# Performance work log

Hardware: AMD Instinct MI355X
Metric: run time of the kernel (lower is better)

The kernel has to match this reference:

```python
import jax, jax.numpy as jnp
import numpy as np

NUM_WIRES = 4
NUM_LAYERS = 2
BATCH = 1_048_576


def _rz(theta):
    # diag(e^{-i t/2}, e^{+i t/2})
    e = jnp.exp(-0.5j * theta.astype(jnp.complex64))
    z = jnp.zeros((), jnp.complex64)
    return jnp.stack([jnp.stack([e, z]), jnp.stack([z, jnp.conj(e)])])


def _rx(theta):
    c = jnp.cos(0.5 * theta).astype(jnp.complex64)
    s = (-1j * jnp.sin(0.5 * theta)).astype(jnp.complex64)
    return jnp.stack([jnp.stack([c, s]), jnp.stack([s, c])])


def _apply_1q(state, U, w):
    # state: (B,2,2,2,2); apply 2x2 unitary U on wire w (axis w+1)
    s = jnp.moveaxis(state, w + 1, -1)
    s = jnp.einsum('...i,ji->...j', s, U)
    return jnp.moveaxis(s, -1, w + 1)


def _cnot(state, c, t):
    # flip target axis where control bit == 1
    s = jnp.moveaxis(state, (c + 1, t + 1), (-2, -1))
    s = jnp.stack([s[..., 0, :], s[..., 1, ::-1]], axis=-2)
    return jnp.moveaxis(s, (-2, -1), (c + 1, t + 1))


def _circuit(x, params):
    # RY(x_i)|0> per wire gives product state [cos(x_i/2), sin(x_i/2)]
    h = 0.5 * x
    a = jnp.stack([jnp.cos(h), jnp.sin(h)], axis=-1).astype(jnp.complex64)  # (B,4,2)
    state = jnp.einsum('bi,bj,bk,bl->bijkl', a[:, 0], a[:, 1], a[:, 2], a[:, 3])
    for layer in range(NUM_LAYERS):
        for w in range(NUM_WIRES):
            # RZ then RX on wire w, fused into one 2x2 unitary
            U = _rx(params[layer, w, 1]) @ _rz(params[layer, w, 0])
            state = _apply_1q(state, U, w)
        for w in range(NUM_WIRES - 1):
            state = _cnot(state, w, w + 1)
        state = _cnot(state, NUM_WIRES - 1, 0)
    probs = state.real ** 2 + state.imag ** 2  # (B,2,2,2,2)
    evs = []
    for w in range(NUM_WIRES):
        axes = tuple(ax for ax in range(1, NUM_WIRES + 1) if ax != w + 1)
        p = jnp.sum(probs, axis=axes)  # (B,2) marginal of wire w
        evs.append(p[:, 0] - p[:, 1])  # <Z_w>
    return jnp.stack(evs, axis=-1)  # (B,4)


def setup_inputs() -> dict:
    key = jax.random.key(0)
    k1, k2 = jax.random.split(key)
    x = jax.random.normal(k1, (BATCH, NUM_WIRES), dtype=jnp.float32)
    params = jax.random.normal(k2, (NUM_LAYERS, NUM_WIRES, 2), dtype=jnp.float32)
    return {"x": x, "params": params}


def reference(x, params):
    return _circuit(x, params)
```

## Files before the change

kernel.cpp:

```cpp
#include <hip/hip_runtime.h>
#include <math.h>

#define PI_F 3.14159265358979323846f


typedef __attribute__((address_space(4))) const float cfloat;

__global__ void gate_prep(const float* __restrict__ params, float* __restrict__ g) {
    __shared__ float L[324];
    const int tid = threadIdx.x;

    if (tid < 81) {
        const int t3 = tid % 3, t2 = (tid / 3) % 3, t1 = (tid / 9) % 3, t0 = tid / 27;
        const float xg[3] = {0.f, PI_F, 0.5f * PI_F};
        const float xs[4] = {xg[t0], xg[t1], xg[t2], xg[t3]};

        float zr[16], zi[16];
        {
            float c[4], s[4];
            for (int k = 0; k < 4; ++k) { c[k] = cosf(0.5f * xs[k]); s[k] = sinf(0.5f * xs[k]); }
            for (int i = 0; i < 16; ++i) {
                zr[i] = ((i & 8) ? s[0] : c[0]) * ((i & 4) ? s[1] : c[1]) *
                        ((i & 2) ? s[2] : c[2]) * ((i & 1) ? s[3] : c[3]);
                zi[i] = 0.f;
            }
        }
        for (int layer = 0; layer < 2; ++layer) {
            for (int w = 0; w < 4; ++w) {
                const float p0 = params[(layer * 4 + w) * 2 + 0];
                const float p1 = params[(layer * 4 + w) * 2 + 1];
                const float cz = cosf(0.5f * p0), sz = sinf(0.5f * p0);
                const float cx = cosf(0.5f * p1), sx = sinf(0.5f * p1);
                const float u00r = cx * cz,  u00i = -cx * sz;
                const float u01r = sx * sz,  u01i = -sx * cz;
                const float u10r = -sx * sz, u10i = -sx * cz;
                const float u11r = cx * cz,  u11i = cx * sz;
                const int M = 8 >> w;
                for (int i = 0; i < 16; ++i) {
                    if (!(i & M)) {
                        const int j = i | M;
                        const float ar = zr[i], ai = zi[i], br = zr[j], bi = zi[j];
                        zr[i] = u00r * ar - u00i * ai + u01r * br - u01i * bi;
                        zi[i] = u00r * ai + u00i * ar + u01r * bi + u01i * br;
                        zr[j] = u10r * ar - u10i * ai + u11r * br - u11i * bi;
                        zi[j] = u10r * ai + u10i * ar + u11r * bi + u11i * br;
                    }
                }
            }
            const int cm[4] = {8, 4, 2, 1}, tmm[4] = {4, 2, 1, 8};
            for (int kk = 0; kk < 4; ++kk)
                for (int i = 0; i < 16; ++i)
                    if ((i & cm[kk]) && !(i & tmm[kk])) {
                        const int j = i | tmm[kk];
                        float t;
                        t = zr[i]; zr[i] = zr[j]; zr[j] = t;
                        t = zi[i]; zi[i] = zi[j]; zi[j] = t;
                    }
        }
        float p[16];
        for (int i = 0; i < 16; ++i) p[i] = zr[i] * zr[i] + zi[i] * zi[i];
        const int wm[4] = {8, 4, 2, 1};
        for (int w = 0; w < 4; ++w) {
            float e = 0.f;
            for (int i = 0; i < 16; ++i) e += (i & wm[w]) ? -p[i] : p[i];
            L[w * 81 + tid] = e;
        }
    }
    __syncthreads();

    const int strides[4] = {27, 9, 3, 1};
    for (int d = 0; d < 4; ++d) {
        const int S = strides[d];
        if (tid < 108) {
            const int w = tid & 3, grp = tid >> 2;
            const int base = w * 81 + (grp / S) * (3 * S) + (grp % S);
            const float v0 = L[base], v1 = L[base + S], v2 = L[base + 2 * S];
            const float a0 = 0.5f * (v0 + v1);
            const float a1 = 0.5f * (v0 - v1);
            L[base] = a0;
            L[base + S] = a1;
            L[base + 2 * S] = v2 - a0;
        }
        __syncthreads();
    }

    for (int k = tid; k < 324; k += blockDim.x) {
        g[k] = L[(k & 3) * 81 + (k >> 2)];
    }
}

__global__ __launch_bounds__(256) void qsim_kernel(const float* __restrict__ x,
                                                   const float* __restrict__ gf,
                                                   float* __restrict__ out, int batch) {
    const int b = blockIdx.x * 256 + threadIdx.x;
    if (b >= batch) return;

    cfloat* T = (cfloat*)gf;

    const float4 xv = reinterpret_cast<const float4*>(x)[b];
    float c[4], s[4];
    __sincosf(xv.x, &s[0], &c[0]);
    __sincosf(xv.y, &s[1], &c[1]);
    __sincosf(xv.z, &s[2], &c[2]);
    __sincosf(xv.w, &s[3], &c[3]);

    float u[9];
    u[1] = c[3];        u[2] = s[3];
    u[3] = c[2];        u[6] = s[2];
    u[4] = c[2] * c[3]; u[5] = c[2] * s[3];
    u[7] = s[2] * c[3]; u[8] = s[2] * s[3];

    float ev[4];
#pragma unroll
    for (int t0 = 0; t0 < 3; ++t0) {
        float o1[4];
#pragma unroll
        for (int t1 = 0; t1 < 3; ++t1) {
            cfloat* Tp = T + (t0 * 3 + t1) * 36;
            float inner[4];
#pragma unroll
            for (int w = 0; w < 4; ++w) inner[w] = Tp[w];
#pragma unroll
            for (int p = 1; p < 9; ++p)
#pragma unroll
                for (int w = 0; w < 4; ++w)
                    inner[w] = fmaf(u[p], Tp[p * 4 + w], inner[w]);

            if (t1 == 0) {
#pragma unroll
                for (int w = 0; w < 4; ++w) o1[w] = inner[w];
            } else if (t1 == 1) {
#pragma unroll
                for (int w = 0; w < 4; ++w) o1[w] = fmaf(c[1], inner[w], o1[w]);
            } else {
#pragma unroll
                for (int w = 0; w < 4; ++w) o1[w] = fmaf(s[1], inner[w], o1[w]);
            }
        }
        if (t0 == 0) {
#pragma unroll
            for (int w = 0; w < 4; ++w) ev[w] = o1[w];
        } else if (t0 == 1) {
#pragma unroll
            for (int w = 0; w < 4; ++w) ev[w] = fmaf(c[0], o1[w], ev[w]);
        } else {
#pragma unroll
            for (int w = 0; w < 4; ++w) ev[w] = fmaf(s[0], o1[w], ev[w]);
        }
    }

    reinterpret_cast<float4*>(out)[b] = make_float4(ev[0], ev[1], ev[2], ev[3]);
}

extern "C" void kernel_launch(void* const* d_in, const int* in_sizes, int n_in,
                              void* d_out, int out_size, void* d_ws, size_t ws_size,
                              hipStream_t stream) {
    const float* x = (const float*)d_in[0];
    const float* params = (const float*)d_in[1];
    float* out = (float*)d_out;
    float* g = (float*)d_ws;
    const int batch = in_sizes[0] / 4;

    gate_prep<<<1, 128, 0, stream>>>(params, g);
    const int blocks = (batch + 255) / 256;
    qsim_kernel<<<blocks, 256, 0, stream>>>(x, g, out, batch);
}
```

Measured before the change: 89.65 us.

## Process two batch elements per thread and loop over tensor blocks with vector loads

Each thread now evaluates two samples, so every coefficient of the precomputed 324-float tensor it reads is used for two FMAs instead of one. The fully unrolled 9-block contraction becomes a non-unrolled loop that loads each 36-float block as float4 vectors through ordinary global pointers instead of constant-address-space scalar loads. This is meant to cut coefficient load traffic and instruction count per sample. In exchange it launches half as many blocks, adds loop overhead and per-iteration weight selects, and raises register use.

Result: no change. 90.41 us (+0.9%).

```diff
diff --git a/kernel.cpp b/kernel.cpp
--- a/kernel.cpp
+++ b/kernel.cpp
@@ -3,8 +3,6 @@
 
 #define PI_F 3.14159265358979323846f
 
-
-typedef __attribute__((address_space(4))) const float cfloat;
 
 __global__ void gate_prep(const float* __restrict__ params, float* __restrict__ g) {
     __shared__ float L[324];
@@ -90,66 +88,86 @@
 }
 
 __global__ __launch_bounds__(256) void qsim_kernel(const float* __restrict__ x,
-                                                   const float* __restrict__ gf,
+                                                   const float* __restrict__ T,
                                                    float* __restrict__ out, int batch) {
-    const int b = blockIdx.x * 256 + threadIdx.x;
-    if (b >= batch) return;
+    const int tid = threadIdx.x;
+    const int i0 = blockIdx.x * 512 + tid;
+    const int i1 = i0 + 256;
 
-    cfloat* T = (cfloat*)gf;
+    const float4 xa = (i0 < batch) ? reinterpret_cast<const float4*>(x)[i0]
+                                   : make_float4(0.f, 0.f, 0.f, 0.f);
+    const float4 xb = (i1 < batch) ? reinterpret_cast<const float4*>(x)[i1]
+                                   : make_float4(0.f, 0.f, 0.f, 0.f);
 
-    const float4 xv = reinterpret_cast<const float4*>(x)[b];
-    float c[4], s[4];
-    __sincosf(xv.x, &s[0], &c[0]);
-    __sincosf(xv.y, &s[1], &c[1]);
-    __sincosf(xv.z, &s[2], &c[2]);
-    __sincosf(xv.w, &s[3], &c[3]);
+    float cA[4], sA[4], cB[4], sB[4];
+    __sincosf(xa.x, &sA[0], &cA[0]);
+    __sincosf(xa.y, &sA[1], &cA[1]);
+    __sincosf(xa.z, &sA[2], &cA[2]);
+    __sincosf(xa.w, &sA[3], &cA[3]);
+    __sincosf(xb.x, &sB[0], &cB[0]);
+    __sincosf(xb.y, &sB[1], &cB[1]);
+    __sincosf(xb.z, &sB[2], &cB[2]);
+    __sincosf(xb.w, &sB[3], &cB[3]);
 
-    float u[9];
-    u[1] = c[3];        u[2] = s[3];
-    u[3] = c[2];        u[6] = s[2];
-    u[4] = c[2] * c[3]; u[5] = c[2] * s[3];
-    u[7] = s[2] * c[3]; u[8] = s[2] * s[3];
+    float uA[9], uB[9];
+    uA[1] = cA[3];          uA[2] = sA[3];
+    uA[3] = cA[2];          uA[6] = sA[2];
+    uA[4] = cA[2] * cA[3];  uA[5] = cA[2] * sA[3];
+    uA[7] = sA[2] * cA[3];  uA[8] = sA[2] * sA[3];
+    uB[1] = cB[3];          uB[2] = sB[3];
+    uB[3] = cB[2];          uB[6] = sB[2];
+    uB[4] = cB[2] * cB[3];  uB[5] = cB[2] * sB[3];
+    uB[7] = sB[2] * cB[3];  uB[8] = sB[2] * sB[3];
 
-    float ev[4];
+    float evA[4] = {0.f, 0.f, 0.f, 0.f};
+    float evB[4] = {0.f, 0.f, 0.f, 0.f};
+
+    const float* Tp = T;
+    int t0 = 0, t1 = 0;
+#pragma clang loop unroll(disable)
+    for (int q = 0; q < 9; ++q) {
+        float Tc[36];
 #pragma unroll
-    for (int t0 = 0; t0 < 3; ++t0) {
-        float o1[4];
+        for (int k = 0; k < 9; ++k) {
+            const float4 v = reinterpret_cast<const float4*>(Tp)[k];
+            Tc[4 * k + 0] = v.x;
+            Tc[4 * k + 1] = v.y;
+            Tc[4 * k + 2] = v.z;
+            Tc[4 * k + 3] = v.w;
+        }
+
+        float inA[4], inB[4];
 #pragma unroll
-        for (int t1 = 0; t1 < 3; ++t1) {
-            cfloat* Tp = T + (t0 * 3 + t1) * 36;
-            float inner[4];
+        for (int w = 0; w < 4; ++w) { inA[w] = Tc[w]; inB[w] = Tc[w]; }
 #pragma unroll
-            for (int w = 0; w < 4; ++w) inner[w] = Tp[w];
+        for (int p = 1; p < 9; ++p)
 #pragma unroll
-            for (int p = 1; p < 9; ++p)
+            for (int w = 0; w < 4; ++w) {
+                inA[w] = fmaf(uA[p], Tc[p * 4 + w], inA[w]);
+                inB[w] = fmaf(uB[p], Tc[p * 4 + w], inB[w]);
+            }
+
+        const float w0A = (t0 == 0) ? 1.0f : ((t0 == 1) ? cA[0] : sA[0]);
+        const float w1A = (t1 == 0) ? 1.0f : ((t1 == 1) ? cA[1] : sA[1]);
+        const float w0B = (t0 == 0) ? 1.0f : ((t0 == 1) ? cB[0] : sB[0]);
+        const float w1B = (t1 == 0) ? 1.0f : ((t1 == 1) ? cB[1] : sB[1]);
+        const float wA = w0A * w1A;
+        const float wB = w0B * w1B;
+
 #pragma unroll
-                for (int w = 0; w < 4; ++w)
-                    inner[w] = fmaf(u[p], Tp[p * 4 + w], inner[w]);
+        for (int w = 0; w < 4; ++w) {
+            evA[w] = fmaf(wA, inA[w], evA[w]);
+            evB[w] = fmaf(wB, inB[w], evB[w]);
+        }
 
-            if (t1 == 0) {
-#pragma unroll
-                for (int w = 0; w < 4; ++w) o1[w] = inner[w];
-            } else if (t1 == 1) {
-#pragma unroll
-                for (int w = 0; w < 4; ++w) o1[w] = fmaf(c[1], inner[w], o1[w]);
-            } else {
-#pragma unroll
-                for (int w = 0; w < 4; ++w) o1[w] = fmaf(s[1], inner[w], o1[w]);
-            }
-        }
-        if (t0 == 0) {
-#pragma unroll
-            for (int w = 0; w < 4; ++w) ev[w] = o1[w];
-        } else if (t0 == 1) {
-#pragma unroll
-            for (int w = 0; w < 4; ++w) ev[w] = fmaf(c[0], o1[w], ev[w]);
-        } else {
-#pragma unroll
-            for (int w = 0; w < 4; ++w) ev[w] = fmaf(s[0], o1[w], ev[w]);
-        }
+        Tp += 36;
+        if (++t1 == 3) { t1 = 0; ++t0; }
     }
 
-    reinterpret_cast<float4*>(out)[b] = make_float4(ev[0], ev[1], ev[2], ev[3]);
+    if (i0 < batch)
+        reinterpret_cast<float4*>(out)[i0] = make_float4(evA[0], evA[1], evA[2], evA[3]);
+    if (i1 < batch)
+        reinterpret_cast<float4*>(out)[i1] = make_float4(evB[0], evB[1], evB[2], evB[3]);
 }
 
 extern "C" void kernel_launch(void* const* d_in, const int* in_sizes, int n_in,
@@ -162,6 +180,6 @@
     const int batch = in_sizes[0] / 4;
 
     gate_prep<<<1, 128, 0, stream>>>(params, g);
-    const int blocks = (batch + 255) / 256;
+    const int blocks = (batch + 511) / 512;
     qsim_kernel<<<blocks, 256, 0, stream>>>(x, g, out, batch);
 }
```
